# Performance work log

Hardware: AMD Instinct MI355X
Metric: run time of the kernel (lower is better)

## Reference

```python
import jax, jax.numpy as jnp
import numpy as np

N = 8192      # total nodes
B = 64        # graphs in batch
NPG = 128     # nodes per graph (equal-size graphs; idx sorted)
D_IN = 256
H = 256       # hidden_dim (d_model)
NH = 4        # nhead
HD = H // NH
FF = 2 * H    # dim_feedforward
NC = 16       # n_class


def setup_inputs() -> dict:
    key = jax.random.key(0)
    ks = jax.random.split(key, 16)
    def rn(k, shp, scale=0.05):
        return jax.random.normal(k, shp, jnp.float32) * scale
    inp = {}
    inp["x_in"] = jax.random.normal(ks[0], (N, D_IN), jnp.float32)
    # scale adjacency so each row sums ~1 to keep activations well-conditioned
    inp["adj"] = jax.random.uniform(ks[1], (N, N), jnp.float32) * (2.0 / N)
    inp["idx"] = jnp.repeat(jnp.arange(B, dtype=jnp.int32), NPG)
    inp["cum_nodes"] = jnp.full((B,), NPG, jnp.int32)
    # fc1
    inp["W1"] = rn(ks[2], (D_IN, H)); inp["b1"] = jnp.zeros((H,), jnp.float32)
    # transformer encoder layer (eval mode, dropout inactive)
    inp["in_w"] = rn(ks[3], (H, 3 * H)); inp["in_b"] = jnp.zeros((3 * H,), jnp.float32)
    inp["out_w"] = rn(ks[4], (H, H));    inp["out_b"] = jnp.zeros((H,), jnp.float32)
    inp["ln1_s"] = jnp.ones((H,), jnp.float32); inp["ln1_b"] = jnp.zeros((H,), jnp.float32)
    inp["ff1_w"] = rn(ks[5], (H, FF)); inp["ff1_b"] = jnp.zeros((FF,), jnp.float32)
    inp["ff2_w"] = rn(ks[6], (FF, H)); inp["ff2_b"] = jnp.zeros((H,), jnp.float32)
    inp["ln2_s"] = jnp.ones((H,), jnp.float32); inp["ln2_b"] = jnp.zeros((H,), jnp.float32)
    # fc3 / fc4
    inp["W3"] = rn(ks[7], (H, H));  inp["b3"] = jnp.zeros((H,), jnp.float32)
    inp["W4"] = rn(ks[8], (H, NC)); inp["b4"] = jnp.zeros((NC,), jnp.float32)
    return inp


def _layer_norm(x, s, b):
    mu = x.mean(-1, keepdims=True)
    xc = x - mu
    return xc * jax.lax.rsqrt((xc * xc).mean(-1, keepdims=True) + 1e-5) * s + b


def reference(x_in, adj, idx, cum_nodes, W1, b1, in_w, in_b, out_w, out_b,
              ln1_s, ln1_b, ff1_w, ff1_b, ff2_w, ff2_b, ln2_s, ln2_b,
              W3, b3, W4, b4):
    Bg = cum_nodes.shape[0]
    n = x_in.shape[0] // Bg  # equal-size graphs -> pad_sequence == reshape
    x = x_in @ W1 + b1                      # fc1
    x = jax.nn.relu(adj @ x)                # adjacency message passing
    p = x.reshape(Bg, n, H)                 # pack: idx is sorted, graphs equal size
    # --- TransformerEncoderLayer (post-LN, relu FFN, eval mode) ---
    qkv = p @ in_w + in_b                   # [B, n, 3H]
    q, k, v = jnp.split(qkv, 3, axis=-1)
    q = q.reshape(Bg, n, NH, HD); k = k.reshape(Bg, n, NH, HD); v = v.reshape(Bg, n, NH, HD)
    att = jax.nn.softmax(jnp.einsum('bqhd,bkhd->bhqk', q, k) / np.sqrt(HD), axis=-1)
    o = jnp.einsum('bhqk,bkhd->bqhd', att, v).reshape(Bg, n, H) @ out_w + out_b
    y = _layer_norm(p + o, ln1_s, ln1_b)
    ff = jax.nn.relu(y @ ff1_w + ff1_b) @ ff2_w + ff2_b
    y = _layer_norm(y + ff, ln2_s, ln2_b)
    # --- unpack + scatter-add pooling over graphs ---
    flat = y.reshape(Bg * n, H)
    pooled = jax.ops.segment_sum(flat, idx, num_segments=Bg)  # [B, H]
    out = jax.nn.relu(pooled @ W3 + b3) @ W4 + b4
    return jax.nn.log_softmax(out, axis=-1)
```

## Files before the change

kernel.cpp:

```cpp
#include <hip/hip_runtime.h>

typedef float fx4 __attribute__((ext_vector_type(4)));
typedef short s16x8 __attribute__((ext_vector_type(8)));
typedef short s16x4 __attribute__((ext_vector_type(4)));
typedef unsigned short ushort_t;

__device__ __forceinline__ short f2bf(float f) {
  union { float f; unsigned u; } v; v.f = f;
  unsigned r = v.u + 0x7FFFu + ((v.u >> 16) & 1u);
  return (short)(r >> 16);
}

__device__ __forceinline__ float bf2f(short h) {
  union { float f; unsigned u; } v;
  v.u = ((unsigned)(unsigned short)h) << 16;
  return v.f;
}

__device__ __forceinline__ unsigned cvt_pk_bf16(float a, float b) {
  unsigned r;
  asm("v_cvt_pk_bf16_f32 %0, %1, %2" : "=v"(r) : "v"(a), "v"(b));
  return r;
}

__device__ __forceinline__ s16x8 cvt8(fx4 a, fx4 b) {
  union { s16x8 s; unsigned u[4]; } w;
  w.u[0] = cvt_pk_bf16(a[0], a[1]);
  w.u[1] = cvt_pk_bf16(a[2], a[3]);
  w.u[2] = cvt_pk_bf16(b[0], b[1]);
  w.u[3] = cvt_pk_bf16(b[2], b[3]);
  return w.s;
}

__device__ __forceinline__ void gload16(const void* g, void* l) {
  __builtin_amdgcn_global_load_lds(
      (const __attribute__((address_space(1))) unsigned int*)g,
      (__attribute__((address_space(3))) unsigned int*)l, 16, 0, 0);
}

__global__ __launch_bounds__(256) void prep_kernel(
    const float* __restrict__ W1, const float* __restrict__ in_w,
    const float* __restrict__ out_w, const float* __restrict__ ff1_w,
    const float* __restrict__ ff2_w,
    ushort_t* __restrict__ W1t, ushort_t* __restrict__ in_wT,
    ushort_t* __restrict__ out_wT, ushort_t* __restrict__ ff1t,
    ushort_t* __restrict__ ff2t) {
  const int bid = blockIdx.x, t = threadIdx.x;
  const float* W; ushort_t* Wt; int K, N, base;
  if (bid < 256)       { W = W1;    Wt = W1t;    K = 256; N = 256; base = 0; }
  else if (bid < 1024) { W = in_w;  Wt = in_wT;  K = 256; N = 768; base = 256; }
  else if (bid < 1280) { W = out_w; Wt = out_wT; K = 256; N = 256; base = 1024; }
  else if (bid < 1792) { W = ff1_w; Wt = ff1t;   K = 256; N = 512; base = 1280; }
  else                 { W = ff2_w; Wt = ff2t;   K = 512; N = 256; base = 1792; }
  const int idx = (bid - base) * 256 + t;
  const int k = idx / N, n = idx - k * N;
  Wt[(size_t)n * K + k] = (ushort_t)f2bf(W[idx]);
}

template<int MF, bool AF32, int OUTM, bool RELU, bool RES>
__global__ __launch_bounds__(256) void gemm2(
    const void* __restrict__ Av, const ushort_t* __restrict__ Bt,
    const float* __restrict__ bias, const float* __restrict__ res,
    const float* __restrict__ lns, const float* __restrict__ lnb,
    float* __restrict__ Cf, ushort_t* __restrict__ Cb,
    int M, int N, int K, int kLen) {
  constexpr int BM = MF * 16;
  __shared__ __align__(16) ushort_t Asm[2][BM * 64];
  __shared__ __align__(16) ushort_t Bsm[256 * 64];
  const int t = threadIdx.x, lane = t & 63, wave = t >> 6;
  const int bm = blockIdx.y * BM;
  const int bn = (OUTM == 5) ? 0 : blockIdx.x * 256;
  const int kOff = (OUTM == 5) ? blockIdx.x * kLen : 0;
  const int wn = wave * 64, fr = lane & 15, fq = lane >> 4;
  const int NT = kLen >> 6;
  const int x0 = ((fq) ^ (fr & 7)) * 8;
  const int x1 = ((4 + fq) ^ (fr & 7)) * 8;
  fx4 acc[MF][4] = {};

  const int gl = lane >> 3, gc = lane & 7;
  const int gsw = (gc ^ gl) * 8;
  const ushort_t* Bgl =
      Bt + (size_t)(bn + wave * 64 + gl) * K + kOff + gsw;
  const ushort_t* Agl =
      (const ushort_t*)Av + (size_t)(bm + wave * (BM / 4) + gl) * K + kOff + gsw;
  constexpr int TPR = 256 / BM;
  const int arow = t / TPR;
  const int ac0 = (t % TPR) * (BM / 4);
  const float* Afp = (const float*)Av + (size_t)(bm + arow) * K + kOff + ac0;
  fx4 R[MF / 2][2];

  auto issueB = [&](int kt) {
    #pragma unroll
    for (int i = 0; i < 8; ++i)
      gload16(Bgl + (size_t)i * 8 * K + kt * 64, &Bsm[wave * 4096 + i * 512]);
  };
  auto issueAg = [&](int buf, int kt) {
    #pragma unroll
    for (int i = 0; i < MF / 2; ++i)
      gload16(Agl + (size_t)i * 8 * K + kt * 64,
              &Asm[buf][wave * (BM * 16) + i * 512]);
  };
  auto loadR = [&](int kt) {
    #pragma unroll
    for (int w = 0; w < MF / 2; ++w) {
      R[w][0] = *(const fx4*)(Afp + kt * 64 + w * 8);
      R[w][1] = *(const fx4*)(Afp + kt * 64 + w * 8 + 4);
    }
  };
  auto writeA = [&](int buf) {
    #pragma unroll
    for (int w = 0; w < MF / 2; ++w) {
      const int cs = ((ac0 >> 3) + w) ^ (arow & 7);
      *(s16x8*)&Asm[buf][arow * 64 + cs * 8] = cvt8(R[w][0], R[w][1]);
    }
  };

  if constexpr (AF32) { loadR(0); issueB(0); writeA(0); loadR(1); }
  else { issueAg(0, 0); issueB(0); }
  __syncthreads();

  #pragma unroll 1
  for (int kt = 0; kt < NT; ++kt) {
    const int cur = kt & 1;
    s16x8 b0[4], b1[4], a0[MF], a1[MF];
    #pragma unroll
    for (int nf = 0; nf < 4; ++nf) {
      b0[nf] = *(const s16x8*)&Bsm[(wn + nf * 16 + fr) * 64 + x0];
      b1[nf] = *(const s16x8*)&Bsm[(wn + nf * 16 + fr) * 64 + x1];
    }
    #pragma unroll
    for (int mf = 0; mf < MF; ++mf)
      a0[mf] = *(const s16x8*)&Asm[cur][(mf * 16 + fr) * 64 + x0];
    asm volatile("s_waitcnt lgkmcnt(0)" ::: "memory");
    if (kt + 1 < NT) {
      if constexpr (AF32) {
        writeA(cur ^ 1);
        if (kt + 2 < NT) loadR(kt + 2);
        issueB(kt + 1);
      } else {
        issueAg(cur ^ 1, kt + 1);
        issueB(kt + 1);
      }
    }
    #pragma unroll
    for (int mf = 0; mf < MF; ++mf)
      #pragma unroll
      for (int nf = 0; nf < 4; ++nf)
        acc[mf][nf] = __builtin_amdgcn_mfma_f32_16x16x32_bf16(
            a0[mf], b0[nf], acc[mf][nf], 0, 0, 0);
    #pragma unroll
    for (int mf = 0; mf < MF; ++mf)
      a1[mf] = *(const s16x8*)&Asm[cur][(mf * 16 + fr) * 64 + x1];
    #pragma unroll
    for (int mf = 0; mf < MF; ++mf)
      #pragma unroll
      for (int nf = 0; nf < 4; ++nf)
        acc[mf][nf] = __builtin_amdgcn_mfma_f32_16x16x32_bf16(
            a1[mf], b1[nf], acc[mf][nf], 0, 0, 0);
    __syncthreads();
  }

  if constexpr (OUTM == 3) {
    #pragma unroll
    for (int mf = 0; mf < MF; ++mf)
      #pragma unroll
      for (int nf = 0; nf < 4; ++nf) {
        const int col = bn + wn + nf * 16 + fr;
        const float bb = bias[col];
        s16x4 w;
        #pragma unroll
        for (int r = 0; r < 4; ++r) w[r] = f2bf(acc[mf][nf][r] + bb);
        *(s16x4*)&Cb[(size_t)col * M + bm + mf * 16 + fq * 4] = w;
      }
  } else if constexpr (OUTM == 5) {
    ushort_t* po = Cb + (size_t)blockIdx.x * ((size_t)M * 256);
    #pragma unroll
    for (int mf = 0; mf < MF; ++mf)
      #pragma unroll
      for (int nf = 0; nf < 4; ++nf)
        #pragma unroll
        for (int r = 0; r < 4; ++r)
          po[(size_t)(bm + mf * 16 + fq * 4 + r) * 256 + wn + nf * 16 + fr] =
              (ushort_t)f2bf(acc[mf][nf][r]);
  } else if constexpr (OUTM == 4) {
    float* red_s = (float*)&Asm[0][0];
    float* red_q = red_s + 128;
    float vv[MF][4][4];
    #pragma unroll
    for (int mf = 0; mf < MF; ++mf)
      #pragma unroll
      for (int nf = 0; nf < 4; ++nf) {
        const int col = wn + nf * 16 + fr;
        #pragma unroll
        for (int r = 0; r < 4; ++r) {
          const int row = bm + mf * 16 + fq * 4 + r;
          float x = acc[mf][nf][r] + bias[col];
          if constexpr (RES) x += res[(size_t)row * 256 + col];
          vv[mf][nf][r] = x;
        }
      }
    #pragma unroll
    for (int mf = 0; mf < MF; ++mf)
      #pragma unroll
      for (int r = 0; r < 4; ++r) {
        float s = vv[mf][0][r] + vv[mf][1][r] + vv[mf][2][r] + vv[mf][3][r];
        float q = vv[mf][0][r] * vv[mf][0][r] + vv[mf][1][r] * vv[mf][1][r] +
                  vv[mf][2][r] * vv[mf][2][r] + vv[mf][3][r] * vv[mf][3][r];
        #pragma unroll
        for (int off = 1; off < 16; off <<= 1) {
          s += __shfl_xor(s, off, 64);
          q += __shfl_xor(q, off, 64);
        }
        if (fr == 0) {
          red_s[(mf * 16 + fq * 4 + r) * 4 + wave] = s;
          red_q[(mf * 16 + fq * 4 + r) * 4 + wave] = q;
        }
      }
    __syncthreads();
    #pragma unroll
    for (int mf = 0; mf < MF; ++mf)
      #pragma unroll
      for (int r = 0; r < 4; ++r) {
        const int rl = mf * 16 + fq * 4 + r;
        const float st = red_s[rl * 4] + red_s[rl * 4 + 1] +
                         red_s[rl * 4 + 2] + red_s[rl * 4 + 3];
        const float qt = red_q[rl * 4] + red_q[rl * 4 + 1] +
                         red_q[rl * 4 + 2] + red_q[rl * 4 + 3];
        const float mu = st * (1.f / 256.f);
        const float var = qt * (1.f / 256.f) - mu * mu;
        const float rr = rsqrtf(var + 1e-5f);
        const int row = bm + rl;
        #pragma unroll
        for (int nf = 0; nf < 4; ++nf) {
          const int col = wn + nf * 16 + fr;
          const float o = (vv[mf][nf][r] - mu) * rr * lns[col] + lnb[col];
          Cf[(size_t)row * 256 + col] = o;
          Cb[(size_t)row * 256 + col] = (ushort_t)f2bf(o);
        }
      }
  } else {
    #pragma unroll
    for (int mf = 0; mf < MF; ++mf)
      #pragma unroll
      for (int nf = 0; nf < 4; ++nf) {
        const int col = bn + wn + nf * 16 + fr;
        const float bb = bias[col];
        #pragma unroll
        for (int r = 0; r < 4; ++r) {
          const int row = bm + mf * 16 + fq * 4 + r;
          float x = acc[mf][nf][r] + bb;
          if constexpr (RES) x += res[(size_t)row * N + col];
          if constexpr (RELU) x = fmaxf(x, 0.f);
          if constexpr (OUTM == 0 || OUTM == 2) Cf[(size_t)row * N + col] = x;
          if constexpr (OUTM == 1 || OUTM == 2)
            Cb[(size_t)row * N + col] = (ushort_t)f2bf(x);
        }
      }
  }
}

__global__ __launch_bounds__(256) void relu_reduce8(
    const ushort_t* __restrict__ part, float* __restrict__ p,
    ushort_t* __restrict__ pb) {
  const size_t i = ((size_t)blockIdx.x * 256 + threadIdx.x) * 8;
  const size_t S = 8192ull * 256ull;
  float a[8] = {};
  #pragma unroll
  for (int j = 0; j < 8; ++j) {
    const s16x8 v = *(const s16x8*)(part + j * S + i);
    #pragma unroll
    for (int c = 0; c < 8; ++c) a[c] += bf2f(v[c]);
  }
  fx4 v0, v1;
  #pragma unroll
  for (int c = 0; c < 4; ++c) {
    v0[c] = fmaxf(a[c], 0.f);
    v1[c] = fmaxf(a[c + 4], 0.f);
  }
  *(fx4*)(p + i) = v0;
  *(fx4*)(p + i + 4) = v1;
  s16x8 w;
  #pragma unroll
  for (int c = 0; c < 4; ++c) { w[c] = f2bf(v0[c]); w[c + 4] = f2bf(v1[c]); }
  *(s16x8*)(pb + i) = w;
}

__global__ __launch_bounds__(256) void att_fused(
    const float* __restrict__ qkv, ushort_t* __restrict__ attout) {
  __shared__ float k_s[128][68];
  __shared__ float v_s[128][68];
  __shared__ float s_s[128][129];
  __shared__ float pm[2][128];
  __shared__ float ps[2][128];
  const int bh = blockIdx.x, b = bh >> 2, h = bh & 3;
  const int t = threadIdx.x;
  const float* base = qkv + (size_t)b * 128 * 768 + h * 64;
  for (int e = t; e < 128 * 64; e += 256) {
    const int n = e >> 6, d = e & 63;
    k_s[n][d] = base[(size_t)n * 768 + 256 + d];
    v_s[n][d] = base[(size_t)n * 768 + 512 + d];
  }
  const int row = t & 127, kh = t >> 7;
  fx4 qr[16];
  const fx4* qrow = (const fx4*)(base + (size_t)row * 768);
  #pragma unroll
  for (int c = 0; c < 16; ++c) qr[c] = qrow[c];
  __syncthreads();
  float m = -1e30f;
  for (int j = 0; j < 64; ++j) {
    const int jj = kh * 64 + j;
    const fx4* kr = (const fx4*)&k_s[jj][0];
    float s0 = 0.f, s1 = 0.f, s2 = 0.f, s3 = 0.f;
    #pragma unroll
    for (int c = 0; c < 16; c += 4) {
      fx4 k0 = kr[c], k1 = kr[c + 1], k2 = kr[c + 2], k3 = kr[c + 3];
      s0 += qr[c][0]*k0[0] + qr[c][1]*k0[1] + qr[c][2]*k0[2] + qr[c][3]*k0[3];
      s1 += qr[c+1][0]*k1[0] + qr[c+1][1]*k1[1] + qr[c+1][2]*k1[2] + qr[c+1][3]*k1[3];
      s2 += qr[c+2][0]*k2[0] + qr[c+2][1]*k2[1] + qr[c+2][2]*k2[2] + qr[c+2][3]*k2[3];
      s3 += qr[c+3][0]*k3[0] + qr[c+3][1]*k3[1] + qr[c+3][2]*k3[2] + qr[c+3][3]*k3[3];
    }
    const float s = (s0 + s1 + s2 + s3) * 0.125f;
    s_s[row][jj] = s;
    m = fmaxf(m, s);
  }
  pm[kh][row] = m;
  __syncthreads();
  const float m2 = fmaxf(pm[0][row], pm[1][row]);
  float sum = 0.f;
  for (int j = 0; j < 64; ++j) {
    const int jj = kh * 64 + j;
    const float e = __expf(s_s[row][jj] - m2);
    s_s[row][jj] = e;
    sum += e;
  }
  ps[kh][row] = sum;
  __syncthreads();
  const int row2 = t >> 1, dh = (t & 1) * 32;
  const float inv = 1.f / (ps[0][row2] + ps[1][row2]);
  fx4 acc4[8] = {};
  for (int k = 0; k < 128; ++k) {
    const float e = s_s[row2][k];
    const fx4* vr = (const fx4*)&v_s[k][dh];
    #pragma unroll
    for (int c = 0; c < 8; ++c) acc4[c] += e * vr[c];
  }
  ushort_t* orow = attout + (size_t)(b * 128 + row2) * 256 + h * 64 + dh;
  #pragma unroll
  for (int c = 0; c < 8; ++c) {
    const fx4 v = acc4[c] * inv;
    s16x4 w;
    #pragma unroll
    for (int j = 0; j < 4; ++j) w[j] = f2bf(v[j]);
    *(s16x4*)(orow + c * 4) = w;
  }
}

__global__ __launch_bounds__(256) void pool_kernel(
    const float* __restrict__ y2, float* __restrict__ pooled4) {
  const int bq = blockIdx.x;
  const int b = bq >> 2, q = bq & 3, h = threadIdx.x;
  const float* pb = y2 + ((size_t)b * 128 + q * 32) * 256 + h;
  float s = 0.f;
  for (int n = 0; n < 32; ++n) s += pb[(size_t)n * 256];
  pooled4[(size_t)bq * 256 + h] = s;
}

__global__ __launch_bounds__(256) void head_kernel(
    const float* __restrict__ pooled4, const float* __restrict__ W3,
    const float* __restrict__ b3, const float* __restrict__ W4,
    const float* __restrict__ b4, float* __restrict__ out) {
  __shared__ float sp[256];
  __shared__ float t1[256];
  __shared__ float logits[16];
  const int b = blockIdx.x, h = threadIdx.x;
  sp[h] = pooled4[(size_t)(b * 4 + 0) * 256 + h] +
          pooled4[(size_t)(b * 4 + 1) * 256 + h] +
          pooled4[(size_t)(b * 4 + 2) * 256 + h] +
          pooled4[(size_t)(b * 4 + 3) * 256 + h];
  __syncthreads();
  float a = b3[h];
  for (int k = 0; k < 256; ++k) a += sp[k] * W3[k * 256 + h];
  t1[h] = fmaxf(a, 0.f);
  __syncthreads();
  if (h < 16) {
    float o = b4[h];
    for (int j = 0; j < 256; ++j) o += t1[j] * W4[j * 16 + h];
    logits[h] = o;
  }
  __syncthreads();
  if (h < 16) {
    float mm = -1e30f;
    #pragma unroll
    for (int c = 0; c < 16; ++c) mm = fmaxf(mm, logits[c]);
    float se = 0.f;
    #pragma unroll
    for (int c = 0; c < 16; ++c) se += __expf(logits[c] - mm);
    out[b * 16 + h] = logits[h] - mm - logf(se);
  }
}

extern "C" void kernel_launch(void* const* d_in, const int* in_sizes, int n_in,
                              void* d_out, int out_size, void* d_ws, size_t ws_size,
                              hipStream_t stream) {
  const float* x_in  = (const float*)d_in[0];
  const float* adj   = (const float*)d_in[1];
  const float* W1    = (const float*)d_in[4];
  const float* b1    = (const float*)d_in[5];
  const float* in_w  = (const float*)d_in[6];
  const float* in_b  = (const float*)d_in[7];
  const float* out_w = (const float*)d_in[8];
  const float* out_b = (const float*)d_in[9];
  const float* ln1_s = (const float*)d_in[10];
  const float* ln1_b = (const float*)d_in[11];
  const float* ff1_w = (const float*)d_in[12];
  const float* ff1_b = (const float*)d_in[13];
  const float* ff2_w = (const float*)d_in[14];
  const float* ff2_b = (const float*)d_in[15];
  const float* ln2_s = (const float*)d_in[16];
  const float* ln2_b = (const float*)d_in[17];
  const float* W3    = (const float*)d_in[18];
  const float* b3    = (const float*)d_in[19];
  const float* W4    = (const float*)d_in[20];
  const float* b4    = (const float*)d_in[21];
  char* ws = (char*)d_ws;
  const size_t MB = 1ull << 20;
  ushort_t* xT      = (ushort_t*)(ws);
  ushort_t* W1t     = (ushort_t*)(ws + 4 * MB);
  ushort_t* in_wT   = (ushort_t*)(ws + 4 * MB + 131072);
  ushort_t* out_wT  = (ushort_t*)(ws + 4 * MB + 524288);
  ushort_t* ff1t    = (ushort_t*)(ws + 4 * MB + 655360);
  ushort_t* ff2t    = (ushort_t*)(ws + 4 * MB + 917504);
  float*    p       = (float*)(ws + 8 * MB);
  ushort_t* p_bf    = (ushort_t*)(ws + 16 * MB);
  float*    qkvb    = (float*)(ws + 20 * MB);
  ushort_t* attout  = (ushort_t*)(ws + 44 * MB);
  float*    y       = (float*)(ws + 48 * MB);
  ushort_t* y_bf    = (ushort_t*)(ws + 56 * MB);
  ushort_t* f1_bf   = (ushort_t*)(ws + 60 * MB);
  float*    y2      = (float*)(ws + 68 * MB);
  float*    pooled4 = (float*)(ws + 76 * MB);
  ushort_t* part    = (ushort_t*)(ws + 77 * MB);
  float*    outp    = (float*)d_out;
  (void)in_sizes; (void)n_in; (void)out_size; (void)ws_size;

  prep_kernel<<<2304, 256, 0, stream>>>(W1, in_w, out_w, ff1_w, ff2_w,
                                        W1t, in_wT, out_wT, ff1t, ff2t);
  gemm2<2, true, 3, false, false><<<dim3(1, 256), 256, 0, stream>>>(
      x_in, W1t, b1, nullptr, nullptr, nullptr, nullptr, xT,
      8192, 256, 256, 256);
  gemm2<4, true, 5, false, false><<<dim3(8, 128), 256, 0, stream>>>(
      adj, xT, nullptr, nullptr, nullptr, nullptr, nullptr, part,
      8192, 256, 8192, 1024);
  relu_reduce8<<<1024, 256, 0, stream>>>(part, p, p_bf);
  gemm2<4, false, 0, false, false><<<dim3(3, 128), 256, 0, stream>>>(
      p_bf, in_wT, in_b, nullptr, nullptr, nullptr, qkvb, nullptr,
      8192, 768, 256, 256);
  att_fused<<<256, 256, 0, stream>>>(qkvb, attout);
  gemm2<2, false, 4, false, true><<<dim3(1, 256), 256, 0, stream>>>(
      attout, out_wT, out_b, p, ln1_s, ln1_b, y, y_bf,
      8192, 256, 256, 256);
  gemm2<4, false, 1, true, false><<<dim3(2, 128), 256, 0, stream>>>(
      y_bf, ff1t, ff1_b, nullptr, nullptr, nullptr, nullptr, f1_bf,
      8192, 512, 256, 256);
  gemm2<2, false, 4, false, true><<<dim3(1, 256), 256, 0, stream>>>(
      f1_bf, ff2t, ff2_b, y, ln2_s, ln2_b, y2, y_bf,
      8192, 256, 512, 512);
  pool_kernel<<<256, 256, 0, stream>>>(y2, pooled4);
  head_kernel<<<64, 256, 0, stream>>>(pooled4, W3, b3, W4, b4, outp);
}
```

Measured before the change: 222.0 us.

## Fuse out-proj, LN1, FFN, LN2 and pooling into one tail kernel; bf16 QKV

Replaces the out-projection GEMM, the two FFN GEMMs, both layer norms and the pooling kernel with a single tail_kernel. Each 32-row block keeps y and the FFN hidden activations in shared memory and reduces its rows straight into pooled partial sums, so the fp32 y, y2 and bf16 intermediates never go through global memory. The QKV GEMM now writes bf16 instead of fp32, and attention reads bf16 and converts to float. In exchange, the tail kernel runs only 256 blocks with a large LDS footprint and serialized weight streaming, and QKV loses precision.

```diff
diff --git a/kernel.cpp b/kernel.cpp
--- a/kernel.cpp
+++ b/kernel.cpp
@@ -182,62 +182,6 @@
         for (int r = 0; r < 4; ++r)
           po[(size_t)(bm + mf * 16 + fq * 4 + r) * 256 + wn + nf * 16 + fr] =
               (ushort_t)f2bf(acc[mf][nf][r]);
-  } else if constexpr (OUTM == 4) {
-    float* red_s = (float*)&Asm[0][0];
-    float* red_q = red_s + 128;
-    float vv[MF][4][4];
-    #pragma unroll
-    for (int mf = 0; mf < MF; ++mf)
-      #pragma unroll
-      for (int nf = 0; nf < 4; ++nf) {
-        const int col = wn + nf * 16 + fr;
-        #pragma unroll
-        for (int r = 0; r < 4; ++r) {
-          const int row = bm + mf * 16 + fq * 4 + r;
-          float x = acc[mf][nf][r] + bias[col];
-          if constexpr (RES) x += res[(size_t)row * 256 + col];
-          vv[mf][nf][r] = x;
-        }
-      }
-    #pragma unroll
-    for (int mf = 0; mf < MF; ++mf)
-      #pragma unroll
-      for (int r = 0; r < 4; ++r) {
-        float s = vv[mf][0][r] + vv[mf][1][r] + vv[mf][2][r] + vv[mf][3][r];
-        float q = vv[mf][0][r] * vv[mf][0][r] + vv[mf][1][r] * vv[mf][1][r] +
-                  vv[mf][2][r] * vv[mf][2][r] + vv[mf][3][r] * vv[mf][3][r];
-        #pragma unroll
-        for (int off = 1; off < 16; off <<= 1) {
-          s += __shfl_xor(s, off, 64);
-          q += __shfl_xor(q, off, 64);
-        }
-        if (fr == 0) {
-          red_s[(mf * 16 + fq * 4 + r) * 4 + wave] = s;
-          red_q[(mf * 16 + fq * 4 + r) * 4 + wave] = q;
-        }
-      }
-    __syncthreads();
-    #pragma unroll
-    for (int mf = 0; mf < MF; ++mf)
-      #pragma unroll
-      for (int r = 0; r < 4; ++r) {
-        const int rl = mf * 16 + fq * 4 + r;
-        const float st = red_s[rl * 4] + red_s[rl * 4 + 1] +
-                         red_s[rl * 4 + 2] + red_s[rl * 4 + 3];
-        const float qt = red_q[rl * 4] + red_q[rl * 4 + 1] +
-                         red_q[rl * 4 + 2] + red_q[rl * 4 + 3];
-        const float mu = st * (1.f / 256.f);
-        const float var = qt * (1.f / 256.f) - mu * mu;
-        const float rr = rsqrtf(var + 1e-5f);
-        const int row = bm + rl;
-        #pragma unroll
-        for (int nf = 0; nf < 4; ++nf) {
-          const int col = wn + nf * 16 + fr;
-          const float o = (vv[mf][nf][r] - mu) * rr * lns[col] + lnb[col];
-          Cf[(size_t)row * 256 + col] = o;
-          Cb[(size_t)row * 256 + col] = (ushort_t)f2bf(o);
-        }
-      }
   } else {
     #pragma unroll
     for (int mf = 0; mf < MF; ++mf)
@@ -286,7 +230,7 @@
 }
 
 __global__ __launch_bounds__(256) void att_fused(
-    const float* __restrict__ qkv, ushort_t* __restrict__ attout) {
+    const ushort_t* __restrict__ qkv, ushort_t* __restrict__ attout) {
   __shared__ float k_s[128][68];
   __shared__ float v_s[128][68];
   __shared__ float s_s[128][129];
@@ -294,17 +238,30 @@
   __shared__ float ps[2][128];
   const int bh = blockIdx.x, b = bh >> 2, h = bh & 3;
   const int t = threadIdx.x;
-  const float* base = qkv + (size_t)b * 128 * 768 + h * 64;
-  for (int e = t; e < 128 * 64; e += 256) {
-    const int n = e >> 6, d = e & 63;
-    k_s[n][d] = base[(size_t)n * 768 + 256 + d];
-    v_s[n][d] = base[(size_t)n * 768 + 512 + d];
+  const ushort_t* qb = qkv + (size_t)b * 128 * 768 + h * 64;
+  for (int u = t; u < 1024; u += 256) {
+    const int n = u >> 3, d8 = (u & 7) * 8;
+    const s16x8 kk = *(const s16x8*)(qb + (size_t)n * 768 + 256 + d8);
+    const s16x8 vv = *(const s16x8*)(qb + (size_t)n * 768 + 512 + d8);
+    #pragma unroll
+    for (int c = 0; c < 8; ++c) {
+      k_s[n][d8 + c] = bf2f(kk[c]);
+      v_s[n][d8 + c] = bf2f(vv[c]);
+    }
   }
   const int row = t & 127, kh = t >> 7;
   fx4 qr[16];
-  const fx4* qrow = (const fx4*)(base + (size_t)row * 768);
-  #pragma unroll
-  for (int c = 0; c < 16; ++c) qr[c] = qrow[c];
+  {
+    const s16x8* q8 = (const s16x8*)(qb + (size_t)row * 768);
+    #pragma unroll
+    for (int j = 0; j < 8; ++j) {
+      const s16x8 qv = q8[j];
+      qr[2*j][0] = bf2f(qv[0]); qr[2*j][1] = bf2f(qv[1]);
+      qr[2*j][2] = bf2f(qv[2]); qr[2*j][3] = bf2f(qv[3]);
+      qr[2*j+1][0] = bf2f(qv[4]); qr[2*j+1][1] = bf2f(qv[5]);
+      qr[2*j+1][2] = bf2f(qv[6]); qr[2*j+1][3] = bf2f(qv[7]);
+    }
+  }
   __syncthreads();
   float m = -1e30f;
   for (int j = 0; j < 64; ++j) {
@@ -355,14 +312,269 @@
   }
 }
 
-__global__ __launch_bounds__(256) void pool_kernel(
-    const float* __restrict__ y2, float* __restrict__ pooled4) {
-  const int bq = blockIdx.x;
-  const int b = bq >> 2, q = bq & 3, h = threadIdx.x;
-  const float* pb = y2 + ((size_t)b * 128 + q * 32) * 256 + h;
-  float s = 0.f;
-  for (int n = 0; n < 32; ++n) s += pb[(size_t)n * 256];
-  pooled4[(size_t)bq * 256 + h] = s;
+__global__ __launch_bounds__(256) void tail_kernel(
+    const ushort_t* __restrict__ attout, const ushort_t* __restrict__ out_wT,
+    const float* __restrict__ out_b, const float* __restrict__ p_res,
+    const float* __restrict__ ln1_s, const float* __restrict__ ln1_b,
+    const ushort_t* __restrict__ ff1t, const float* __restrict__ ff1_b,
+    const ushort_t* __restrict__ ff2t, const float* __restrict__ ff2_b,
+    const float* __restrict__ ln2_s, const float* __restrict__ ln2_b,
+    float* __restrict__ pooled4) {
+  __shared__ __align__(16) ushort_t Asm[2][32 * 64];
+  __shared__ __align__(16) ushort_t Bsm[256 * 64];
+  __shared__ __align__(16) ushort_t y_s[32 * 256];
+  __shared__ __align__(16) ushort_t f1_s[32 * 512];
+  __shared__ float red_s[128], red_q[128];
+  const int t = threadIdx.x, lane = t & 63, wave = t >> 6;
+  const int bq = blockIdx.x, bm = bq * 32;
+  const int wn = wave * 64, fr = lane & 15, fq = lane >> 4;
+  const int x0 = (fq ^ (fr & 7)) * 8, x1 = ((4 + fq) ^ (fr & 7)) * 8;
+  const int gl = lane >> 3, gc = lane & 7, gsw = (gc ^ gl) * 8;
+
+  fx4 acc[2][4] = {};
+  {
+    const ushort_t* Agl = attout + (size_t)(bm + wave * 8 + gl) * 256 + gsw;
+    const ushort_t* Bgl = out_wT + (size_t)(wave * 64 + gl) * 256 + gsw;
+    auto issueA = [&](int buf, int kt) {
+      gload16(Agl + kt * 64, &Asm[buf][wave * 512]);
+    };
+    auto issueB = [&](int kt) {
+      #pragma unroll
+      for (int i = 0; i < 8; ++i)
+        gload16(Bgl + (size_t)i * 8 * 256 + kt * 64,
+                &Bsm[wave * 4096 + i * 512]);
+    };
+    issueA(0, 0); issueB(0);
+    __syncthreads();
+    #pragma unroll 1
+    for (int kt = 0; kt < 4; ++kt) {
+      const int cur = kt & 1;
+      s16x8 b0[4], b1[4], a0[2], a1[2];
+      #pragma unroll
+      for (int nf = 0; nf < 4; ++nf) {
+        b0[nf] = *(const s16x8*)&Bsm[(wn + nf * 16 + fr) * 64 + x0];
+        b1[nf] = *(const s16x8*)&Bsm[(wn + nf * 16 + fr) * 64 + x1];
+      }
+      #pragma unroll
+      for (int mf = 0; mf < 2; ++mf) {
+        a0[mf] = *(const s16x8*)&Asm[cur][(mf * 16 + fr) * 64 + x0];
+        a1[mf] = *(const s16x8*)&Asm[cur][(mf * 16 + fr) * 64 + x1];
+      }
+      asm volatile("s_waitcnt lgkmcnt(0)" ::: "memory");
+      if (kt < 3) { issueA(cur ^ 1, kt + 1); issueB(kt + 1); }
+      #pragma unroll
+      for (int mf = 0; mf < 2; ++mf)
+        #pragma unroll
+        for (int nf = 0; nf < 4; ++nf) {
+          acc[mf][nf] = __builtin_amdgcn_mfma_f32_16x16x32_bf16(
+              a0[mf], b0[nf], acc[mf][nf], 0, 0, 0);
+          acc[mf][nf] = __builtin_amdgcn_mfma_f32_16x16x32_bf16(
+              a1[mf], b1[nf], acc[mf][nf], 0, 0, 0);
+        }
+      __syncthreads();
+    }
+  }
+  float yv[2][4][4];
+  #pragma unroll
+  for (int mf = 0; mf < 2; ++mf)
+    #pragma unroll
+    for (int nf = 0; nf < 4; ++nf) {
+      const int col = wn + nf * 16 + fr;
+      #pragma unroll
+      for (int r = 0; r < 4; ++r) {
+        const int row = bm + mf * 16 + fq * 4 + r;
+        yv[mf][nf][r] = acc[mf][nf][r] + out_b[col] +
+                        p_res[(size_t)row * 256 + col];
+      }
+    }
+  {
+    #pragma unroll
+    for (int mf = 0; mf < 2; ++mf)
+      #pragma unroll
+      for (int r = 0; r < 4; ++r) {
+        float s = yv[mf][0][r] + yv[mf][1][r] + yv[mf][2][r] + yv[mf][3][r];
+        float q = yv[mf][0][r]*yv[mf][0][r] + yv[mf][1][r]*yv[mf][1][r] +
+                  yv[mf][2][r]*yv[mf][2][r] + yv[mf][3][r]*yv[mf][3][r];
+        #pragma unroll
+        for (int off = 1; off < 16; off <<= 1) {
+          s += __shfl_xor(s, off, 64);
+          q += __shfl_xor(q, off, 64);
+        }
+        if (fr == 0) {
+          red_s[(mf * 16 + fq * 4 + r) * 4 + wave] = s;
+          red_q[(mf * 16 + fq * 4 + r) * 4 + wave] = q;
+        }
+      }
+    __syncthreads();
+    #pragma unroll
+    for (int mf = 0; mf < 2; ++mf)
+      #pragma unroll
+      for (int r = 0; r < 4; ++r) {
+        const int rl = mf * 16 + fq * 4 + r;
+        const float st = red_s[rl*4] + red_s[rl*4+1] + red_s[rl*4+2] + red_s[rl*4+3];
+        const float qt = red_q[rl*4] + red_q[rl*4+1] + red_q[rl*4+2] + red_q[rl*4+3];
+        const float mu = st * (1.f / 256.f);
+        const float rr = rsqrtf(qt * (1.f / 256.f) - mu * mu + 1e-5f);
+        #pragma unroll
+        for (int nf = 0; nf < 4; ++nf) {
+          const int col = wn + nf * 16 + fr;
+          const float o = (yv[mf][nf][r] - mu) * rr * ln1_s[col] + ln1_b[col];
+          yv[mf][nf][r] = o;
+          y_s[rl * 256 + ((col >> 3) ^ (rl & 7)) * 8 + (col & 7)] =
+              (ushort_t)f2bf(o);
+        }
+      }
+  }
+  __syncthreads();
+
+  #pragma unroll 1
+  for (int ng = 0; ng < 2; ++ng) {
+    const ushort_t* Bgl = ff1t + (size_t)(ng * 256 + wave * 64 + gl) * 256 + gsw;
+    auto issueB = [&](int kt) {
+      #pragma unroll
+      for (int i = 0; i < 8; ++i)
+        gload16(Bgl + (size_t)i * 8 * 256 + kt * 64,
+                &Bsm[wave * 4096 + i * 512]);
+    };
+    fx4 a2[2][4] = {};
+    issueB(0);
+    #pragma unroll 1
+    for (int kt = 0; kt < 4; ++kt) {
+      asm volatile("s_waitcnt vmcnt(0)" ::: "memory");
+      s16x8 b0[4], b1[4], a0[2], a1[2];
+      #pragma unroll
+      for (int nf = 0; nf < 4; ++nf) {
+        b0[nf] = *(const s16x8*)&Bsm[(wn + nf * 16 + fr) * 64 + x0];
+        b1[nf] = *(const s16x8*)&Bsm[(wn + nf * 16 + fr) * 64 + x1];
+      }
+      #pragma unroll
+      for (int mf = 0; mf < 2; ++mf) {
+        const int row = mf * 16 + fr;
+        a0[mf] = *(const s16x8*)&y_s[row * 256 + ((kt*8 + fq) ^ (row & 7)) * 8];
+        a1[mf] = *(const s16x8*)&y_s[row * 256 + ((kt*8 + 4 + fq) ^ (row & 7)) * 8];
+      }
+      asm volatile("s_waitcnt lgkmcnt(0)" ::: "memory");
+      if (kt < 3) issueB(kt + 1);
+      #pragma unroll
+      for (int mf = 0; mf < 2; ++mf)
+        #pragma unroll
+        for (int nf = 0; nf < 4; ++nf) {
+          a2[mf][nf] = __builtin_amdgcn_mfma_f32_16x16x32_bf16(
+              a0[mf], b0[nf], a2[mf][nf], 0, 0, 0);
+          a2[mf][nf] = __builtin_amdgcn_mfma_f32_16x16x32_bf16(
+              a1[mf], b1[nf], a2[mf][nf], 0, 0, 0);
+        }
+    }
+    #pragma unroll
+    for (int mf = 0; mf < 2; ++mf)
+      #pragma unroll
+      for (int nf = 0; nf < 4; ++nf) {
+        const int col = ng * 256 + wn + nf * 16 + fr;
+        const float bb = ff1_b[col];
+        #pragma unroll
+        for (int r = 0; r < 4; ++r) {
+          const int rl = mf * 16 + fq * 4 + r;
+          const float x = fmaxf(a2[mf][nf][r] + bb, 0.f);
+          f1_s[rl * 512 + ((col >> 3) ^ (rl & 7)) * 8 + (col & 7)] =
+              (ushort_t)f2bf(x);
+        }
+      }
+  }
+  __syncthreads();
+
+  {
+    const ushort_t* Bgl = ff2t + (size_t)(wave * 64 + gl) * 512 + gsw;
+    auto issueB = [&](int kt) {
+      #pragma unroll
+      for (int i = 0; i < 8; ++i)
+        gload16(Bgl + (size_t)i * 8 * 512 + kt * 64,
+                &Bsm[wave * 4096 + i * 512]);
+    };
+    fx4 a3[2][4] = {};
+    issueB(0);
+    #pragma unroll 1
+    for (int kt = 0; kt < 8; ++kt) {
+      asm volatile("s_waitcnt vmcnt(0)" ::: "memory");
+      s16x8 b0[4], b1[4], a0[2], a1[2];
+      #pragma unroll
+      for (int nf = 0; nf < 4; ++nf) {
+        b0[nf] = *(const s16x8*)&Bsm[(wn + nf * 16 + fr) * 64 + x0];
+        b1[nf] = *(const s16x8*)&Bsm[(wn + nf * 16 + fr) * 64 + x1];
+      }
+      #pragma unroll
+      for (int mf = 0; mf < 2; ++mf) {
+        const int row = mf * 16 + fr;
+        a0[mf] = *(const s16x8*)&f1_s[row * 512 + ((kt*8 + fq) ^ (row & 7)) * 8];
+        a1[mf] = *(const s16x8*)&f1_s[row * 512 + ((kt*8 + 4 + fq) ^ (row & 7)) * 8];
+      }
+      asm volatile("s_waitcnt lgkmcnt(0)" ::: "memory");
+      if (kt < 7) issueB(kt + 1);
+      #pragma unroll
+      for (int mf = 0; mf < 2; ++mf)
+        #pragma unroll
+        for (int nf = 0; nf < 4; ++nf) {
+          a3[mf][nf] = __builtin_amdgcn_mfma_f32_16x16x32_bf16(
+              a0[mf], b0[nf], a3[mf][nf], 0, 0, 0);
+          a3[mf][nf] = __builtin_amdgcn_mfma_f32_16x16x32_bf16(
+              a1[mf], b1[nf], a3[mf][nf], 0, 0, 0);
+        }
+    }
+    float vv[2][4][4];
+    #pragma unroll
+    for (int mf = 0; mf < 2; ++mf)
+      #pragma unroll
+      for (int nf = 0; nf < 4; ++nf) {
+        const int col = wn + nf * 16 + fr;
+        const float bb = ff2_b[col];
+        #pragma unroll
+        for (int r = 0; r < 4; ++r)
+          vv[mf][nf][r] = a3[mf][nf][r] + bb + yv[mf][nf][r];
+      }
+    __syncthreads();
+    #pragma unroll
+    for (int mf = 0; mf < 2; ++mf)
+      #pragma unroll
+      for (int r = 0; r < 4; ++r) {
+        float s = vv[mf][0][r] + vv[mf][1][r] + vv[mf][2][r] + vv[mf][3][r];
+        float q = vv[mf][0][r]*vv[mf][0][r] + vv[mf][1][r]*vv[mf][1][r] +
+                  vv[mf][2][r]*vv[mf][2][r] + vv[mf][3][r]*vv[mf][3][r];
+        #pragma unroll
+        for (int off = 1; off < 16; off <<= 1) {
+          s += __shfl_xor(s, off, 64);
+          q += __shfl_xor(q, off, 64);
+        }
+        if (fr == 0) {
+          red_s[(mf * 16 + fq * 4 + r) * 4 + wave] = s;
+          red_q[(mf * 16 + fq * 4 + r) * 4 + wave] = q;
+        }
+      }
+    __syncthreads();
+    float colsum[4] = {};
+    #pragma unroll
+    for (int mf = 0; mf < 2; ++mf)
+      #pragma unroll
+      for (int r = 0; r < 4; ++r) {
+        const int rl = mf * 16 + fq * 4 + r;
+        const float st = red_s[rl*4] + red_s[rl*4+1] + red_s[rl*4+2] + red_s[rl*4+3];
+        const float qt = red_q[rl*4] + red_q[rl*4+1] + red_q[rl*4+2] + red_q[rl*4+3];
+        const float mu = st * (1.f / 256.f);
+        const float rr = rsqrtf(qt * (1.f / 256.f) - mu * mu + 1e-5f);
+        #pragma unroll
+        for (int nf = 0; nf < 4; ++nf) {
+          const int col = wn + nf * 16 + fr;
+          colsum[nf] += (vv[mf][nf][r] - mu) * rr * ln2_s[col] + ln2_b[col];
+        }
+      }
+    #pragma unroll
+    for (int nf = 0; nf < 4; ++nf) {
+      colsum[nf] += __shfl_xor(colsum[nf], 16, 64);
+      colsum[nf] += __shfl_xor(colsum[nf], 32, 64);
+    }
+    if (lane < 16)
+      #pragma unroll
+      for (int nf = 0; nf < 4; ++nf)
+        pooled4[(size_t)bq * 256 + wn + nf * 16 + fr] = colsum[nf];
+  }
 }
 
 __global__ __launch_bounds__(256) void head_kernel(
@@ -432,14 +644,10 @@
   ushort_t* ff2t    = (ushort_t*)(ws + 4 * MB + 917504);
   float*    p       = (float*)(ws + 8 * MB);
   ushort_t* p_bf    = (ushort_t*)(ws + 16 * MB);
-  float*    qkvb    = (float*)(ws + 20 * MB);
-  ushort_t* attout  = (ushort_t*)(ws + 44 * MB);
-  float*    y       = (float*)(ws + 48 * MB);
-  ushort_t* y_bf    = (ushort_t*)(ws + 56 * MB);
-  ushort_t* f1_bf   = (ushort_t*)(ws + 60 * MB);
-  float*    y2      = (float*)(ws + 68 * MB);
-  float*    pooled4 = (float*)(ws + 76 * MB);
-  ushort_t* part    = (ushort_t*)(ws + 77 * MB);
+  ushort_t* qkv_bf  = (ushort_t*)(ws + 20 * MB);
+  ushort_t* attout  = (ushort_t*)(ws + 32 * MB);
+  float*    pooled4 = (float*)(ws + 36 * MB);
+  ushort_t* part    = (ushort_t*)(ws + 37 * MB);
   float*    outp    = (float*)d_out;
   (void)in_sizes; (void)n_in; (void)out_size; (void)ws_size;
 
@@ -452,19 +660,12 @@
       adj, xT, nullptr, nullptr, nullptr, nullptr, nullptr, part,
       8192, 256, 8192, 1024);
   relu_reduce8<<<1024, 256, 0, stream>>>(part, p, p_bf);
-  gemm2<4, false, 0, false, false><<<dim3(3, 128), 256, 0, stream>>>(
-      p_bf, in_wT, in_b, nullptr, nullptr, nullptr, qkvb, nullptr,
+  gemm2<4, false, 1, false, false><<<dim3(3, 128), 256, 0, stream>>>(
+      p_bf, in_wT, in_b, nullptr, nullptr, nullptr, nullptr, qkv_bf,
       8192, 768, 256, 256);
-  att_fused<<<256, 256, 0, stream>>>(qkvb, attout);
-  gemm2<2, false, 4, false, true><<<dim3(1, 256), 256, 0, stream>>>(
-      attout, out_wT, out_b, p, ln1_s, ln1_b, y, y_bf,
-      8192, 256, 256, 256);
-  gemm2<4, false, 1, true, false><<<dim3(2, 128), 256, 0, stream>>>(
-      y_bf, ff1t, ff1_b, nullptr, nullptr, nullptr, nullptr, f1_bf,
-      8192, 512, 256, 256);
-  gemm2<2, false, 4, false, true><<<dim3(1, 256), 256, 0, stream>>>(
-      f1_bf, ff2t, ff2_b, y, ln2_s, ln2_b, y2, y_bf,
-      8192, 256, 512, 512);
-  pool_kernel<<<256, 256, 0, stream>>>(y2, pooled4);
+  att_fused<<<256, 256, 0, stream>>>(qkv_bf, attout);
+  tail_kernel<<<256, 256, 0, stream>>>(
+      attout, out_wT, out_b, p, ln1_s, ln1_b, ff1t, ff1_b,
+      ff2t, ff2_b, ln2_s, ln2_b, pooled4);
   head_kernel<<<64, 256, 0, stream>>>(pooled4, W3, b3, W4, b4, outp);
 }
```

After: 194.8 us. 12.2% less time.
